# Optimization experiments

Measured on AMD Instinct MI355X. Metric: run time of the kernel, lower is better.

## Reference

```python
import jax, jax.numpy as jnp
import numpy as np

BN_EPS = 1e-5
SQ_EPS = 1e-7
NUM_SAMPLES = 4
NUM_CHILD = 8
DIM_CHILD = 8
NUM_PARENT = 8
DIM_PARENT = 16
ROUTING_ITERS = 3
OFFSET_SCALE = 1.0


def squash(x, axis=-1):
    sq = jnp.sum(x * x, axis=axis, keepdims=True)
    return (sq / (1.0 + sq)) * x / jnp.sqrt(sq + SQ_EPS)


def bilinear_sample(feat, grid):
    # feat: [B,C,H,W], grid: [B,H,W,2] in [-1,1], align_corners=True, zeros padding
    B, C, H, W = feat.shape
    x = (grid[..., 0] + 1.0) * 0.5 * (W - 1)
    y = (grid[..., 1] + 1.0) * 0.5 * (H - 1)
    x0 = jnp.floor(x); y0 = jnp.floor(y)
    x1 = x0 + 1.0; y1 = y0 + 1.0
    wx1 = x - x0; wx0 = 1.0 - wx1
    wy1 = y - y0; wy0 = 1.0 - wy1
    featf = feat.reshape(B, C, H * W)

    def gather(xi, yi):
        valid = (xi >= 0) & (xi <= W - 1) & (yi >= 0) & (yi <= H - 1)
        xc = jnp.clip(xi, 0, W - 1).astype(jnp.int32)
        yc = jnp.clip(yi, 0, H - 1).astype(jnp.int32)
        idx = (yc * W + xc).reshape(B, 1, H * W)
        v = jnp.take_along_axis(featf, idx, axis=2).reshape(B, C, H, W)
        return v * valid[:, None].astype(feat.dtype)

    out = (gather(x0, y0) * (wx0 * wy0)[:, None]
           + gather(x1, y0) * (wx1 * wy0)[:, None]
           + gather(x0, y1) * (wx0 * wy1)[:, None]
           + gather(x1, y1) * (wx1 * wy1)[:, None])
    return out


def setup_inputs() -> dict:
    key = jax.random.key(0)
    ks = jax.random.split(key, 8)
    B, C, H, W = 8, 256, 32, 32
    caps_ch = NUM_CHILD * DIM_CHILD  # 64
    return {
        "x": jax.random.normal(ks[0], (B, C, H, W), jnp.float32),
        "primary_w": jax.random.normal(ks[1], (caps_ch, C), jnp.float32) * 0.05,
        "bn_gamma": jnp.ones((caps_ch,), jnp.float32),
        "bn_beta": jnp.zeros((caps_ch,), jnp.float32),
        "bn_mean": jax.random.normal(ks[2], (caps_ch,), jnp.float32) * 0.1,
        "bn_var": jax.random.uniform(ks[3], (caps_ch,), jnp.float32, 0.5, 1.5),
        "offset_w": jax.random.normal(ks[4], (2 * NUM_SAMPLES, C, 3, 3), jnp.float32) * 0.01,
        "offset_b": jnp.zeros((2 * NUM_SAMPLES,), jnp.float32),
        "routing_W": jax.random.normal(ks[5], (NUM_SAMPLES * NUM_CHILD, NUM_PARENT, DIM_PARENT, DIM_CHILD), jnp.float32) * 0.01,
    }


def reference(x, primary_w, bn_gamma, bn_beta, bn_mean, bn_var, offset_w, offset_b, routing_W):
    B, C, H, W = x.shape
    # --- PrimaryCaps: 1x1 conv + BN(inference) + SiLU + squash over capsule dim ---
    p = jnp.einsum('bchw,oc->bohw', x, primary_w)
    p = (p - bn_mean[None, :, None, None]) / jnp.sqrt(bn_var + BN_EPS)[None, :, None, None]
    p = p * bn_gamma[None, :, None, None] + bn_beta[None, :, None, None]
    p = jax.nn.silu(p)
    child = p.reshape(B, NUM_CHILD, DIM_CHILD, H, W)
    child = squash(child, axis=2)
    child_flat = child.reshape(B, NUM_CHILD * DIM_CHILD, H, W)

    # --- Offset conv 3x3, SAME padding ---
    off = jax.lax.conv_general_dilated(x, offset_w, (1, 1), 'SAME',
                                       dimension_numbers=('NCHW', 'OIHW', 'NCHW'))
    off = off + offset_b[None, :, None, None]
    off = off.reshape(B, NUM_SAMPLES, 2, H, W)
    off = jnp.tanh(off) * OFFSET_SCALE
    scale = jnp.array([max(W - 1, 1) / 2.0, max(H - 1, 1) / 2.0], x.dtype).reshape(1, 1, 2, 1, 1)
    off = off / scale

    ys = jnp.linspace(-1.0, 1.0, H, dtype=x.dtype)
    xs = jnp.linspace(-1.0, 1.0, W, dtype=x.dtype)
    yy, xx = jnp.meshgrid(ys, xs, indexing='ij')
    base = jnp.stack((xx, yy), axis=-1)  # [H,W,2]
    grids = base[None, None] + jnp.transpose(off, (0, 1, 3, 4, 2))  # [B,S,H,W,2]

    sampled = jax.vmap(lambda g: bilinear_sample(child_flat, g),
                       in_axes=1, out_axes=1)(grids)  # [B,S,caps_ch,H,W]
    sampled = sampled.reshape(B, NUM_SAMPLES, NUM_CHILD, DIM_CHILD, H, W)
    sampled = jnp.transpose(sampled, (0, 4, 5, 1, 2, 3))  # [B,H,W,S,NC,DC]
    sampled = sampled.reshape(B * H * W, NUM_SAMPLES * NUM_CHILD, DIM_CHILD)

    # --- Dynamic routing ---
    # u_hat: [M, N_in, N_out, D_out]
    u_hat = jnp.einsum('nodi,mni->mnod', routing_W, sampled)
    M = u_hat.shape[0]
    b = jnp.zeros((M, NUM_SAMPLES * NUM_CHILD, NUM_PARENT), x.dtype)
    v = None
    for it in range(ROUTING_ITERS):
        c = jax.nn.softmax(b, axis=-1)
        s = jnp.einsum('mno,mnod->mod', c, u_hat)
        v = squash(s, axis=-1)
        if it < ROUTING_ITERS - 1:
            b = b + jnp.einsum('mnod,mod->mno', u_hat, v)

    routed = v.reshape(B, H, W, NUM_PARENT, DIM_PARENT)
    out = jnp.transpose(routed, (0, 3, 4, 1, 2)).reshape(B, NUM_PARENT * DIM_PARENT, H, W)
    return out
```

## Files before the change

kernel.cpp:

```cpp
#include <hip/hip_runtime.h>
#include <math.h>

#define HW 1024
#define Hd 32
#define Wd 32
#define Bn 8
#define Cc 256

typedef _Float16 half2_t __attribute__((ext_vector_type(2)));
union F2H { float f; half2_t h; };

static __device__ __forceinline__ float dot2(half2_t a, half2_t b, float c) {
#if __has_builtin(__builtin_amdgcn_fdot2)
    return __builtin_amdgcn_fdot2(a, b, c, false);
#else
    return c + (float)a.x * (float)b.x + (float)a.y * (float)b.y;
#endif
}

template<int CTRL>
static __device__ __forceinline__ float dppx(float v) {
    union { float f; int i; } a, r;
    a.f = v;
    r.i = __builtin_amdgcn_update_dpp(0, a.i, CTRL, 0xF, 0xF, true);
    return r.f;
}

__global__ __launch_bounds__(256) void kTP(const float* __restrict__ x,
        const float* __restrict__ ow, const float* __restrict__ rw,
        float* __restrict__ xt, float* __restrict__ wt2,
        _Float16* __restrict__ wth) {
    __shared__ float tile[64][65];
    int bid = blockIdx.x;
    if (bid < 512) {
        int b = bid >> 6, ct = (bid >> 4) & 3, ht = bid & 15;
        int c0 = ct * 64, hw0 = ht * 64;
        int tr = threadIdx.x >> 6, tc = threadIdx.x & 63;
        const float* xb = x + ((size_t)b * 256 + c0) * 1024 + hw0;
        #pragma unroll
        for (int k = 0; k < 16; ++k) {
            int c = tr + k * 4;
            tile[c][tc] = xb[(size_t)c * 1024 + tc];
        }
        __syncthreads();
        float* xo = xt + ((size_t)b * 1024 + hw0) * 256 + c0;
        #pragma unroll
        for (int k = 0; k < 16; ++k) {
            int hwl = tr + k * 4;
            xo[(size_t)hwl * 256 + tc] = tile[tc][hwl];
        }
    } else if (bid < 584) {
        int t = (bid - 512) * 256 + threadIdx.x;
        int c = t & 255, oc = (t >> 8) & 7, tap = t >> 11;
        wt2[t] = ow[(oc * 256 + c) * 9 + tap];
    } else {
        int t = (bid - 584) * 256 + threadIdx.x;
        int i = t & 7, l = (t >> 3) & 63, j = t >> 9;
        int n = (l & 3) | ((l >> 1) & 0x1C);
        int half = (l >> 2) & 1;
        int o = j >> 4, d = j & 15;
        wth[t] = (_Float16)rw[n * 1024 + half * 512 + o * 128 + d * 8 + i];
    }
}

__global__ __launch_bounds__(256) void kAB(const float* __restrict__ xt,
        const float* __restrict__ pw, const float* __restrict__ gamma,
        const float* __restrict__ beta, const float* __restrict__ mean,
        const float* __restrict__ var, const float* __restrict__ wt2,
        const float* __restrict__ ob, float* __restrict__ child_t,
        float* __restrict__ grids) {
    __shared__ float wl[16384];
    int wid = threadIdx.x >> 6, lane = threadIdx.x & 63;

    if (blockIdx.x < 512) {
        {
            const float4* pw4 = reinterpret_cast<const float4*>(pw);
            #pragma unroll
            for (int k = 0; k < 16; ++k) {
                int f = k * 256 + threadIdx.x;
                float4 v = pw4[f];
                int o = f >> 6, c4 = f & 63;
                *reinterpret_cast<float4*>(
                    wl + c4 * 256 + (((o ^ c4) & 63) << 2)) = v;
            }
        }
        __syncthreads();
        int o = lane;
        float scale = gamma[o] * rsqrtf(var[o] + 1e-5f);
        float mn = mean[o], bt = beta[o];
        const float4* wl4 = reinterpret_cast<const float4*>(wl);
        #pragma unroll
        for (int pp = 0; pp < 4; pp += 2) {
            int m0 = (blockIdx.x * 4 + wid) * 4 + pp;
            const float4* xa = reinterpret_cast<const float4*>(xt + (size_t)m0 * 256);
            const float4* xb = reinterpret_cast<const float4*>(xt + (size_t)(m0 + 1) * 256);
            float a0 = 0.f, a1 = 0.f;
            #pragma unroll 8
            for (int c4 = 0; c4 < 64; ++c4) {
                float4 wv = wl4[c4 * 64 + (lane ^ (c4 & 63))];
                float4 v0 = xa[c4], v1 = xb[c4];
                a0 += wv.x * v0.x + wv.y * v0.y + wv.z * v0.z + wv.w * v0.w;
                a1 += wv.x * v1.x + wv.y * v1.y + wv.z * v1.z + wv.w * v1.w;
            }
            #pragma unroll
            for (int e = 0; e < 2; ++e) {
                float acc = e ? a1 : a0;
                float t = (acc - mn) * scale + bt;
                float s = t / (1.f + expf(-t));
                float sq = s * s;
                sq += __shfl_xor(sq, 1);
                sq += __shfl_xor(sq, 2);
                sq += __shfl_xor(sq, 4);
                float f = (sq / (1.f + sq)) * rsqrtf(sq + 1e-7f);
                child_t[(size_t)(m0 + e) * 64 + o] = s * f;
            }
        }
        return;
    }

    {
        const float4* wt24 = reinterpret_cast<const float4*>(wt2);
        float4* wl4w = reinterpret_cast<float4*>(wl);
        #pragma unroll
        for (int k = 0; k < 16; ++k)
            wl4w[k * 256 + threadIdx.x] = wt24[k * 256 + threadIdx.x];
    }
    __syncthreads();

    int m0 = ((blockIdx.x - 512) * 4 + wid) * 4;
    int b = m0 >> 10, hw0 = m0 & 1023;
    int yy = hw0 >> 5, xx0 = hw0 & 31;
    const float* xb = xt + (size_t)b * HW * 256;

    float acc[4][8];
    #pragma unroll
    for (int px = 0; px < 4; ++px)
        #pragma unroll
        for (int oc = 0; oc < 8; ++oc) acc[px][oc] = 0.f;

    #pragma unroll
    for (int tap = 0; tap < 9; ++tap) {
        int ky = tap / 3 - 1, kx = tap % 3 - 1;
        int yq = yy + ky;
        bool vy = (yq >= 0) && (yq <= Hd - 1);
        float4 xv[4];
        #pragma unroll
        for (int px = 0; px < 4; ++px) {
            int xq = xx0 + px + kx;
            bool ok = vy && (xq >= 0) && (xq <= Wd - 1);
            float4 z; z.x = z.y = z.z = z.w = 0.f;
            xv[px] = ok ? *reinterpret_cast<const float4*>(
                              xb + (size_t)(yq * Wd + xq) * 256 + lane * 4)
                        : z;
        }
        #pragma unroll
        for (int oc = 0; oc < 8; ++oc) {
            float4 wv = (tap < 8)
                ? *reinterpret_cast<const float4*>(wl + (tap * 8 + oc) * 256 + lane * 4)
                : *reinterpret_cast<const float4*>(wt2 + (8 * 8 + oc) * 256 + lane * 4);
            #pragma unroll
            for (int px = 0; px < 4; ++px)
                acc[px][oc] += xv[px].x * wv.x + xv[px].y * wv.y +
                               xv[px].z * wv.z + xv[px].w * wv.w;
        }
    }

    int l0 = lane & 1, l1 = (lane >> 1) & 1;
    int o2 = (lane >> 2) & 1, o3 = (lane >> 3) & 1, o4 = (lane >> 4) & 1;
    float y1[2][8];
    #pragma unroll
    for (int ph = 0; ph < 2; ++ph)
        #pragma unroll
        for (int oc = 0; oc < 8; ++oc) {
            float keep = l0 ? acc[(ph << 1) | 1][oc] : acc[(ph << 1) | 0][oc];
            float send = l0 ? acc[(ph << 1) | 0][oc] : acc[(ph << 1) | 1][oc];
            y1[ph][oc] = keep + dppx<0xB1>(send);
        }
    float y2[8];
    #pragma unroll
    for (int oc = 0; oc < 8; ++oc) {
        float keep = l1 ? y1[1][oc] : y1[0][oc];
        float send = l1 ? y1[0][oc] : y1[1][oc];
        y2[oc] = keep + dppx<0x4E>(send);
    }
    float z4[4];
    #pragma unroll
    for (int oh = 0; oh < 4; ++oh) {
        float keep = o2 ? y2[(oh << 1) | 1] : y2[(oh << 1) | 0];
        float send = o2 ? y2[(oh << 1) | 0] : y2[(oh << 1) | 1];
        z4[oh] = keep + __shfl_xor(send, 4);
    }
    float w2[2];
    #pragma unroll
    for (int oh = 0; oh < 2; ++oh) {
        float keep = o3 ? z4[(oh << 1) | 1] : z4[(oh << 1) | 0];
        float send = o3 ? z4[(oh << 1) | 0] : z4[(oh << 1) | 1];
        w2[oh] = keep + dppx<0x128>(send);
    }
    {
        float keep = o4 ? w2[1] : w2[0];
        float send = o4 ? w2[0] : w2[1];
        float s = keep + __shfl_xor(send, 16);
        s += __shfl_xor(s, 32);
        if (lane < 32) {
            int px = lane & 3, oc = (lane >> 2) & 7;
            float t = tanhf(s + ob[oc]);
            int coord = oc & 1, si = oc >> 1;
            int xx = xx0 + px;
            float base = coord ? (-1.f + yy * (2.f / 31.f))
                               : (-1.f + xx * (2.f / 31.f));
            grids[(size_t)(m0 + px) * 8 + si * 2 + coord] =
                base + t * (1.f / 15.5f);
        }
    }
}

__global__ __launch_bounds__(256, 2) void kD(const float* __restrict__ child_t,
        const float* __restrict__ grids, const _Float16* __restrict__ wth,
        float* __restrict__ out) {
    __shared__ float vband_s[4][128];
    int wid = threadIdx.x >> 6, lane = threadIdx.x & 63;
    float* vband = vband_s[wid];
    int m = blockIdx.x * 4 + wid;
    int b = m >> 10, hw = m & 1023;
    int n = (lane & 3) | ((lane >> 1) & 0x1C);
    int half = (lane >> 2) & 1;
    int si = n >> 3, ch = n & 7;
    int dsl = (n & 1) * 8 + ((n >> 1) & 1) * 4 + ((n >> 2) & 1) * 2 + ((n >> 3) & 1);

    float gx = grids[m * 8 + si * 2 + 0];
    float gy = grids[m * 8 + si * 2 + 1];
    float xf = (gx + 1.f) * 0.5f * 31.f;
    float yf = (gy + 1.f) * 0.5f * 31.f;
    float x0 = floorf(xf), y0 = floorf(yf);
    float wx1 = xf - x0, wx0 = 1.f - wx1;
    float wy1 = yf - y0, wy0 = 1.f - wy1;
    float sf[8] = {0.f, 0.f, 0.f, 0.f, 0.f, 0.f, 0.f, 0.f};
    const float* cb = child_t + (size_t)b * HW * 64 + ch * 8;
    #pragma unroll
    for (int cy = 0; cy < 2; ++cy) {
        float yq = y0 + (float)cy;
        bool vy = (yq >= 0.f) && (yq <= 31.f);
        float wy = cy ? wy1 : wy0;
        #pragma unroll
        for (int cx = 0; cx < 2; ++cx) {
            float xq = x0 + (float)cx;
            bool ok = vy && (xq >= 0.f) && (xq <= 31.f);
            if (!ok) continue;
            float w = wy * (cx ? wx1 : wx0);
            const float* cp = cb + (size_t)((int)yq * Wd + (int)xq) * 64;
            float4 v0 = *reinterpret_cast<const float4*>(cp);
            float4 v1 = *reinterpret_cast<const float4*>(cp + 4);
            sf[0] += w * v0.x; sf[1] += w * v0.y;
            sf[2] += w * v0.z; sf[3] += w * v0.w;
            sf[4] += w * v1.x; sf[5] += w * v1.y;
            sf[6] += w * v1.z; sf[7] += w * v1.w;
        }
    }
    half2_t sh0 = {(_Float16)sf[0], (_Float16)sf[1]};
    half2_t sh1 = {(_Float16)sf[2], (_Float16)sf[3]};
    half2_t sh2 = {(_Float16)sf[4], (_Float16)sf[5]};
    half2_t sh3 = {(_Float16)sf[6], (_Float16)sf[7]};

    float u[4][16];
    const float4* wt4 = reinterpret_cast<const float4*>(wth);
    #pragma unroll
    for (int o = 0; o < 4; ++o) {
        #pragma unroll
        for (int d = 0; d < 16; ++d) {
            float4 wv = wt4[(o * 16 + d) * 64 + lane];
            F2H a0, a1, a2, a3;
            a0.f = wv.x; a1.f = wv.y; a2.f = wv.z; a3.f = wv.w;
            float acc = dot2(a0.h, sh0, 0.f);
            acc = dot2(a1.h, sh1, acc);
            acc = dot2(a2.h, sh2, acc);
            acc = dot2(a3.h, sh3, acc);
            u[o][d] = acc;
        }
    }

    float bl[4] = {0.f, 0.f, 0.f, 0.f};
    #pragma unroll
    for (int it = 0; it < 3; ++it) {
        float ex[4], rs;
        if (it == 0) {
            ex[0] = ex[1] = ex[2] = ex[3] = 1.f;
            rs = 0.125f;
        } else {
            float mx = fmaxf(fmaxf(bl[0], bl[1]), fmaxf(bl[2], bl[3]));
            mx = fmaxf(mx, __shfl_xor(mx, 4));
            float ssum = 0.f;
            #pragma unroll
            for (int k = 0; k < 4; ++k) { ex[k] = expf(bl[k] - mx); ssum += ex[k]; }
            ssum += __shfl_xor(ssum, 4);
            rs = 1.f / ssum;
        }

        float sval[4];
        #pragma unroll
        for (int o = 0; o < 4; ++o) {
            float cc = ex[o] * rs;
            float y[8];
            #pragma unroll
            for (int d = 0; d < 8; ++d) {
                float t = (n & 1) ? cc * u[o][d] : cc * u[o][d + 8];
                float k = (n & 1) ? cc * u[o][d + 8] : cc * u[o][d];
                y[d] = k + dppx<0xB1>(t);
            }
            float z[4];
            #pragma unroll
            for (int d = 0; d < 4; ++d) {
                float t = (n & 2) ? y[d] : y[d + 4];
                float k = (n & 2) ? y[d + 4] : y[d];
                z[d] = k + dppx<0x4E>(t);
            }
            float w2[2];
            #pragma unroll
            for (int d = 0; d < 2; ++d) {
                float t = (n & 4) ? z[d] : z[d + 2];
                float k = (n & 4) ? z[d + 2] : z[d];
                w2[d] = k + dppx<0x128>(t);
            }
            float t4 = (n & 8) ? w2[0] : w2[1];
            float k4 = (n & 8) ? w2[1] : w2[0];
            float s1 = k4 + __shfl_xor(t4, 16);
            s1 += __shfl_xor(s1, 32);
            sval[o] = s1;
        }
        #pragma unroll
        for (int o = 0; o < 4; ++o) {
            float q = sval[o] * sval[o];
            q += dppx<0xB1>(q);
            q += dppx<0x4E>(q);
            q += dppx<0x128>(q);
            q += __shfl_xor(q, 16);
            float f = (q / (1.f + q)) / sqrtf(q + 1e-7f);
            if ((lane & 32) == 0)
                vband[(half * 4 + o) * 16 + dsl] = sval[o] * f;
        }
        if (it < 2) {
            #pragma unroll
            for (int o = 0; o < 4; ++o) {
                const float4* vr = reinterpret_cast<const float4*>(
                    vband + (half * 4 + o) * 16);
                float4 v0 = vr[0], v1 = vr[1], v2 = vr[2], v3 = vr[3];
                float agg = u[o][0] * v0.x + u[o][1] * v0.y +
                            u[o][2] * v0.z + u[o][3] * v0.w +
                            u[o][4] * v1.x + u[o][5] * v1.y +
                            u[o][6] * v1.z + u[o][7] * v1.w +
                            u[o][8] * v2.x + u[o][9] * v2.y +
                            u[o][10] * v2.z + u[o][11] * v2.w +
                            u[o][12] * v3.x + u[o][13] * v3.y +
                            u[o][14] * v3.z + u[o][15] * v3.w;
                bl[o] += agg;
            }
        } else {
            int o_own = lane >> 4;
            int och = half * 4 + o_own;
            int d0 = ((lane & 3) | ((lane >> 1) & 4)) * 2;
            float va = vband[och * 16 + d0 + 0];
            float vb = vband[och * 16 + d0 + 1];
            float* op = out + ((size_t)b * 128 + och * 16) * HW + hw;
            op[(size_t)(d0 + 0) * HW] = va;
            op[(size_t)(d0 + 1) * HW] = vb;
        }
    }
}

extern "C" void kernel_launch(void* const* d_in, const int* in_sizes, int n_in,
                              void* d_out, int out_size, void* d_ws, size_t ws_size,
                              hipStream_t stream) {
    const float* x     = (const float*)d_in[0];
    const float* pw    = (const float*)d_in[1];
    const float* gamma = (const float*)d_in[2];
    const float* beta  = (const float*)d_in[3];
    const float* mean  = (const float*)d_in[4];
    const float* var   = (const float*)d_in[5];
    const float* ow    = (const float*)d_in[6];
    const float* ob    = (const float*)d_in[7];
    const float* rw    = (const float*)d_in[8];
    float* out = (float*)d_out;
    char* ws = (char*)d_ws;
    float*     child_t = (float*)ws;
    float*     grids   = (float*)(ws + 2097152);
    _Float16*  wth     = (_Float16*)(ws + 2359296);
    float*     wt2     = (float*)(ws + 2424832);
    float*     xt      = (float*)(ws + 2498560);

    hipLaunchKernelGGL(kTP, dim3(712), dim3(256), 0, stream,
                       x, ow, rw, xt, wt2, wth);
    hipLaunchKernelGGL(kAB, dim3(1024), dim3(256), 0, stream,
                       xt, pw, gamma, beta, mean, var, wt2, ob,
                       child_t, grids);
    hipLaunchKernelGGL(kD, dim3(2048), dim3(256), 0, stream,
                       child_t, grids, wth, out);
}
```

Measured before the change: 84.33 us.

## Move primary-capsule 1x1 conv into transpose kernel, reading x directly

The primary 1x1 conv + BN + swish + squash stage now runs in the first kernel as extra blocks. Each block loads a 16-pixel slice of x straight from the original NCHW layout into LDS, so it no longer waits on the transposed xt buffer. The offset-conv path stays in its own kernel, so the pipeline now has a larger first kernel and a smaller second one. The aim is better overlap and less dependence on the transpose, at the cost of a bigger LDS allocation (80KB), which may reduce occupancy for the transpose blocks.

```diff
diff --git a/kernel.cpp b/kernel.cpp
--- a/kernel.cpp
+++ b/kernel.cpp
@@ -26,16 +26,21 @@
     return r.f;
 }
 
-__global__ __launch_bounds__(256) void kTP(const float* __restrict__ x,
+__global__ __launch_bounds__(256) void kTPA(const float* __restrict__ x,
         const float* __restrict__ ow, const float* __restrict__ rw,
+        const float* __restrict__ pw, const float* __restrict__ gamma,
+        const float* __restrict__ beta, const float* __restrict__ mean,
+        const float* __restrict__ var,
         float* __restrict__ xt, float* __restrict__ wt2,
-        _Float16* __restrict__ wth) {
-    __shared__ float tile[64][65];
+        _Float16* __restrict__ wth, float* __restrict__ child_t) {
+    __shared__ float lds[20480];
     int bid = blockIdx.x;
+    int tid = threadIdx.x;
     if (bid < 512) {
+        float (*tile)[65] = (float(*)[65])lds;
         int b = bid >> 6, ct = (bid >> 4) & 3, ht = bid & 15;
         int c0 = ct * 64, hw0 = ht * 64;
-        int tr = threadIdx.x >> 6, tc = threadIdx.x & 63;
+        int tr = tid >> 6, tc = tid & 63;
         const float* xb = x + ((size_t)b * 256 + c0) * 1024 + hw0;
         #pragma unroll
         for (int k = 0; k < 16; ++k) {
@@ -50,50 +55,57 @@
             xo[(size_t)hwl * 256 + tc] = tile[tc][hwl];
         }
     } else if (bid < 584) {
-        int t = (bid - 512) * 256 + threadIdx.x;
+        int t = (bid - 512) * 256 + tid;
         int c = t & 255, oc = (t >> 8) & 7, tap = t >> 11;
         wt2[t] = ow[(oc * 256 + c) * 9 + tap];
-    } else {
-        int t = (bid - 584) * 256 + threadIdx.x;
+    } else if (bid < 712) {
+        int t = (bid - 584) * 256 + tid;
         int i = t & 7, l = (t >> 3) & 63, j = t >> 9;
         int n = (l & 3) | ((l >> 1) & 0x1C);
         int half = (l >> 2) & 1;
         int o = j >> 4, d = j & 15;
         wth[t] = (_Float16)rw[n * 1024 + half * 512 + o * 128 + d * 8 + i];
-    }
-}
-
-__global__ __launch_bounds__(256) void kAB(const float* __restrict__ xt,
-        const float* __restrict__ pw, const float* __restrict__ gamma,
-        const float* __restrict__ beta, const float* __restrict__ mean,
-        const float* __restrict__ var, const float* __restrict__ wt2,
-        const float* __restrict__ ob, float* __restrict__ child_t,
-        float* __restrict__ grids) {
-    __shared__ float wl[16384];
-    int wid = threadIdx.x >> 6, lane = threadIdx.x & 63;
-
-    if (blockIdx.x < 512) {
+    } else {
+        float* xs = lds;
+        float* wl = lds + 4096;
         {
             const float4* pw4 = reinterpret_cast<const float4*>(pw);
             #pragma unroll
             for (int k = 0; k < 16; ++k) {
-                int f = k * 256 + threadIdx.x;
+                int f = k * 256 + tid;
                 float4 v = pw4[f];
                 int o = f >> 6, c4 = f & 63;
                 *reinterpret_cast<float4*>(
                     wl + c4 * 256 + (((o ^ c4) & 63) << 2)) = v;
             }
         }
+        int m0b = (bid - 712) * 16;
+        int b = m0b >> 10, hw0 = m0b & 1023;
+        {
+            int c = tid;
+            const float4* xr = reinterpret_cast<const float4*>(
+                x + ((size_t)b * 256 + c) * 1024 + hw0);
+            float4 q0 = xr[0], q1 = xr[1], q2 = xr[2], q3 = xr[3];
+            xs[0 * 256 + c] = q0.x;  xs[1 * 256 + c] = q0.y;
+            xs[2 * 256 + c] = q0.z;  xs[3 * 256 + c] = q0.w;
+            xs[4 * 256 + c] = q1.x;  xs[5 * 256 + c] = q1.y;
+            xs[6 * 256 + c] = q1.z;  xs[7 * 256 + c] = q1.w;
+            xs[8 * 256 + c] = q2.x;  xs[9 * 256 + c] = q2.y;
+            xs[10 * 256 + c] = q2.z; xs[11 * 256 + c] = q2.w;
+            xs[12 * 256 + c] = q3.x; xs[13 * 256 + c] = q3.y;
+            xs[14 * 256 + c] = q3.z; xs[15 * 256 + c] = q3.w;
+        }
         __syncthreads();
+        int wid = tid >> 6, lane = tid & 63;
         int o = lane;
         float scale = gamma[o] * rsqrtf(var[o] + 1e-5f);
         float mn = mean[o], bt = beta[o];
         const float4* wl4 = reinterpret_cast<const float4*>(wl);
         #pragma unroll
         for (int pp = 0; pp < 4; pp += 2) {
-            int m0 = (blockIdx.x * 4 + wid) * 4 + pp;
-            const float4* xa = reinterpret_cast<const float4*>(xt + (size_t)m0 * 256);
-            const float4* xb = reinterpret_cast<const float4*>(xt + (size_t)(m0 + 1) * 256);
+            int lp = wid * 4 + pp;
+            const float4* xa = reinterpret_cast<const float4*>(xs + lp * 256);
+            const float4* xb = reinterpret_cast<const float4*>(xs + (lp + 1) * 256);
             float a0 = 0.f, a1 = 0.f;
             #pragma unroll 8
             for (int c4 = 0; c4 < 64; ++c4) {
@@ -112,12 +124,17 @@
                 sq += __shfl_xor(sq, 2);
                 sq += __shfl_xor(sq, 4);
                 float f = (sq / (1.f + sq)) * rsqrtf(sq + 1e-7f);
-                child_t[(size_t)(m0 + e) * 64 + o] = s * f;
-            }
-        }
-        return;
-    }
-
+                child_t[(size_t)(m0b + lp + e) * 64 + o] = s * f;
+            }
+        }
+    }
+}
+
+__global__ __launch_bounds__(256) void kB(const float* __restrict__ xt,
+        const float* __restrict__ wt2, const float* __restrict__ ob,
+        float* __restrict__ grids) {
+    __shared__ float wl[16384];
+    int wid = threadIdx.x >> 6, lane = threadIdx.x & 63;
     {
         const float4* wt24 = reinterpret_cast<const float4*>(wt2);
         float4* wl4w = reinterpret_cast<float4*>(wl);
@@ -127,7 +144,7 @@
     }
     __syncthreads();
 
-    int m0 = ((blockIdx.x - 512) * 4 + wid) * 4;
+    int m0 = (blockIdx.x * 4 + wid) * 4;
     int b = m0 >> 10, hw0 = m0 & 1023;
     int yy = hw0 >> 5, xx0 = hw0 & 31;
     const float* xb = xt + (size_t)b * HW * 256;
@@ -387,11 +404,11 @@
     float*     wt2     = (float*)(ws + 2424832);
     float*     xt      = (float*)(ws + 2498560);
 
-    hipLaunchKernelGGL(kTP, dim3(712), dim3(256), 0, stream,
-                       x, ow, rw, xt, wt2, wth);
-    hipLaunchKernelGGL(kAB, dim3(1024), dim3(256), 0, stream,
-                       xt, pw, gamma, beta, mean, var, wt2, ob,
-                       child_t, grids);
+    hipLaunchKernelGGL(kTPA, dim3(1224), dim3(256), 0, stream,
+                       x, ow, rw, pw, gamma, beta, mean, var,
+                       xt, wt2, wth, child_t);
+    hipLaunchKernelGGL(kB, dim3(512), dim3(256), 0, stream,
+                       xt, wt2, ob, grids);
     hipLaunchKernelGGL(kD, dim3(2048), dim3(256), 0, stream,
                        child_t, grids, wth, out);
 }
```

Result: faster. 76.20 us (median of 2 runs) (-9.6%).
